# Kernel tuning notes

Hardware: AMD Instinct MI355X
Metric: run time of the kernel (lower is better)

The kernel has to match this reference:

```python
import jax, jax.numpy as jnp
import numpy as np

H = 512
T = 512
B = 32

def _gru_layer(x_tm, mask_tm, W_ih, W_hh, b_ih, b_hh):
    # x_tm: [T, B, H] time-major input; mask_tm: [T, B, 1] bool (t < length)
    # Precompute input projections for all timesteps: [T, B, 3H]
    x_proj = jnp.einsum('tbi,gi->tbg', x_tm, W_ih) + b_ih

    def step(h, inp):
        xp, m = inp                      # xp: [B,3H], m: [B,1]
        hp = h @ W_hh.T + b_hh           # [B,3H]
        xr, xz, xn = jnp.split(xp, 3, axis=-1)
        hr, hz, hn = jnp.split(hp, 3, axis=-1)
        r = jax.nn.sigmoid(xr + hr)
        z = jax.nn.sigmoid(xz + hz)
        n = jnp.tanh(xn + r * hn)
        h_new = (1.0 - z) * n + z * h
        # packed-sequence semantics: hidden frozen past length, output zero past length
        h = jnp.where(m, h_new, h)
        y = jnp.where(m, h_new, jnp.zeros_like(h_new))
        return h, y

    h0 = jnp.zeros((x_tm.shape[1], W_hh.shape[1]), x_tm.dtype)
    _, ys = jax.lax.scan(step, h0, (x_proj, mask_tm))
    return ys  # [T, B, H]


def setup_inputs() -> dict:
    key = jax.random.key(0)
    ks = jax.random.split(key, 12)
    edu_hidden = jax.random.normal(ks[0], (B, T, H), dtype=jnp.float32)
    edu_lengths = jax.random.randint(ks[1], (B,), 1, T + 1)
    edu_lengths = edu_lengths.at[0].set(T)  # pad_packed output length == T
    s = 1.0 / np.sqrt(H)
    def U(k, shape):
        return jax.random.uniform(k, shape, jnp.float32, -s, s)
    return {
        'edu_hidden': edu_hidden,
        'edu_lengths': edu_lengths,
        'W_ih_0': U(ks[2], (3 * H, H)), 'W_hh_0': U(ks[3], (3 * H, H)),
        'b_ih_0': U(ks[4], (3 * H,)),   'b_hh_0': U(ks[5], (3 * H,)),
        'W_ih_1': U(ks[6], (3 * H, H)), 'W_hh_1': U(ks[7], (3 * H, H)),
        'b_ih_1': U(ks[8], (3 * H,)),   'b_hh_1': U(ks[9], (3 * H,)),
    }


def reference(edu_hidden, edu_lengths, W_ih_0, W_hh_0, b_ih_0, b_hh_0,
              W_ih_1, W_hh_1, b_ih_1, b_hh_1):
    # mask[t, b] = t < edu_lengths[b]
    t_idx = jnp.arange(T)
    mask_tm = (t_idx[:, None] < edu_lengths[None, :])[:, :, None]  # [T, B, 1]
    x = jnp.transpose(edu_hidden, (1, 0, 2))  # time-major [T, B, H]
    x = _gru_layer(x, mask_tm, W_ih_0, W_hh_0, b_ih_0, b_hh_0)
    x = _gru_layer(x, mask_tm, W_ih_1, W_hh_1, b_ih_1, b_hh_1)
    return jnp.transpose(x, (1, 0, 2))  # [B, T, H], zeros past each length
```

## Files before the change

kernel.cpp:

```cpp
#include <hip/hip_runtime.h>
#include <cstdint>
#include <cstddef>

#define Hdim 512
#define Tdim 512
#define Bdim 32
#define NWG  256
#define SCAN_THREADS 384

typedef float        f32x4 __attribute__((ext_vector_type(4)));
typedef unsigned int u32x4 __attribute__((ext_vector_type(4)));
typedef unsigned int u32x2 __attribute__((ext_vector_type(2)));

__device__ __forceinline__ float sigmoidf_(float v) {
    return 1.f / (1.f + __expf(-v));
}
__device__ __forceinline__ float tanhf_(float a) {
    float ax = fabsf(a);
    float e  = __expf(-2.f * ax);
    float t  = (1.f - e) / (1.f + e);
    return copysignf(t, a);
}

__global__ void __launch_bounds__(SCAN_THREADS, 1)
gru_scan(const float* __restrict__ xp,
         const float* __restrict__ Whh,
         const float* __restrict__ bhh,
         const int*   __restrict__ lens,
         float*       __restrict__ y,
         u32x2*       hb2,
         int t0, int Tc)
{
    __shared__ float  hlf[4 * Hdim];
    __shared__ float4 part4[16 * 49];
    __shared__ float  dummy_guard[4];

    const int tid = threadIdx.x;
    const int wg  = blockIdx.x;
    const int u   = wg & 31;
    const int bg  = wg >> 5;
    const int j0  = u << 4;
    const int b0  = bg << 2;
    const int rp  = tid >> 4;
    const int kq  = tid & 15;

    float4 w0[8], w1[8];
    {
        int g0 = ((rp >> 4) << 9) + j0 + (rp & 15);
        int r1 = rp + 24;
        int g1 = ((r1 >> 4) << 9) + j0 + (r1 & 15);
        const float* p0 = Whh + ((size_t)g0 << 9) + (kq << 5);
        const float* p1 = Whh + ((size_t)g1 << 9) + (kq << 5);
#pragma unroll
        for (int i = 0; i < 8; ++i) {
            w0[i] = *(const float4*)(p0 + (i << 2));
            w1[i] = *(const float4*)(p1 + (i << 2));
        }
    }

    const bool isGate = tid < 64;
    const int gjl = tid & 15;
    const int gb  = (tid >> 4) & 3;
    const int jg  = j0 + gjl;
    int   glen = 0;
    float bh_r = 0.f, bh_z = 0.f, bh_n = 0.f;
    int holdIdx = 0;
    const float* xpb = nullptr;
    if (isGate) {
        glen = lens[b0 + gb];
        bh_r = bhh[jg];
        bh_z = bhh[512 + jg];
        bh_n = bhh[1024 + jg];
        int L = jg >> 2, c = jg & 3;
        int P = L ^ ((L >> 3) & 7);
        holdIdx = (gb << 9) + (P << 2) + c;
        xpb = xp + (size_t)(b0 + gb) * Tc * 1536;
    }

    const bool isPoll = tid < 256;
    const int  pb  = tid >> 6;
    const int  pL  = (tid & 63) << 1;
    const int  pP0 = pL ^ ((pL >> 3) & 7);
    const int  pP1 = pP0 ^ 1;
    float* lds_w0 = &hlf[(pb << 9) + (pP0 << 2)];
    float* lds_w1 = &hlf[(pb << 9) + (pP1 << 2)];

    float xr = 0.f, xz = 0.f, xn = 0.f;
    if (isGate) {
        xr = xpb[jg];
        xz = xpb[512 + jg];
        xn = xpb[1024 + jg];
    }

    int budget = 1 << 20;

    for (int t = t0; t < t0 + Tc; ++t) {
        const unsigned tg = (unsigned)t;

        if (isPoll) {
            const u32x2* src = hb2 + ((size_t)(t & 1) << 14) + (bg << 11) + (tid << 3);
            u32x4 q0, q1, q2, q3;
            for (;;) {
                asm volatile(
                    "global_load_dwordx4 %0, %4, off sc0 sc1\n\t"
                    "global_load_dwordx4 %1, %4, off offset:16 sc0 sc1\n\t"
                    "global_load_dwordx4 %2, %4, off offset:32 sc0 sc1\n\t"
                    "global_load_dwordx4 %3, %4, off offset:48 sc0 sc1\n\t"
                    "s_waitcnt vmcnt(0)"
                    : "=&v"(q0), "=&v"(q1), "=&v"(q2), "=&v"(q3)
                    : "v"(src) : "memory");
                bool ok = (q0[1] == tg) & (q0[3] == tg) & (q1[1] == tg) & (q1[3] == tg) &
                          (q2[1] == tg) & (q2[3] == tg) & (q3[1] == tg) & (q3[3] == tg);
                if (__all(ok)) break;
                if (--budget < 0) break;
            }
            f32x4 h0 = { __uint_as_float(q0[0]), __uint_as_float(q0[2]),
                         __uint_as_float(q1[0]), __uint_as_float(q1[2]) };
            f32x4 h1 = { __uint_as_float(q2[0]), __uint_as_float(q2[2]),
                         __uint_as_float(q3[0]), __uint_as_float(q3[2]) };
            *(f32x4*)lds_w0 = h0;
            *(f32x4*)lds_w1 = h1;
        }
        float xrn = 0.f, xzn = 0.f, xnn = 0.f;
        if (isGate) {
            int tf = (t + 1 < t0 + Tc) ? (t + 1 - t0) : (t - t0);
            const float* xq = xpb + (size_t)tf * 1536;
            xrn = xq[jg];
            xzn = xq[512 + jg];
            xnn = xq[1024 + jg];
        }
        __syncthreads();

        float acc0[4], acc1[4];
#pragma unroll
        for (int b = 0; b < 4; ++b) {
            const float4* hb = (const float4*)&hlf[b << 9];
            float a0 = 0.f, a1 = 0.f;
#pragma unroll
            for (int i = 0; i < 8; ++i) {
                float4 h = hb[(kq << 3) + (i ^ (kq & 7))];
                a0 = fmaf(w0[i].x, h.x, a0);
                a0 = fmaf(w0[i].y, h.y, a0);
                a0 = fmaf(w0[i].z, h.z, a0);
                a0 = fmaf(w0[i].w, h.w, a0);
                a1 = fmaf(w1[i].x, h.x, a1);
                a1 = fmaf(w1[i].y, h.y, a1);
                a1 = fmaf(w1[i].z, h.z, a1);
                a1 = fmaf(w1[i].w, h.w, a1);
            }
            acc0[b] = a0; acc1[b] = a1;
        }
        part4[kq * 49 + rp]      = make_float4(acc0[0], acc0[1], acc0[2], acc0[3]);
        part4[kq * 49 + rp + 24] = make_float4(acc1[0], acc1[1], acc1[2], acc1[3]);
        __syncthreads();

        if (isGate) {
            const float* part = (const float*)part4;
            float s0 = 0.f, s1 = 0.f, s2 = 0.f;
#pragma unroll
            for (int k = 0; k < 16; ++k) {
                const float* pp = part + (k * 49) * 4;
                s0 += pp[(gjl << 2) + gb];
                s1 += pp[((16 + gjl) << 2) + gb];
                s2 += pp[((32 + gjl) << 2) + gb];
            }
            float hold = hlf[holdIdx];
            float rg = sigmoidf_(xr + s0 + bh_r);
            float zg = sigmoidf_(xz + s1 + bh_z);
            float ng = tanhf_(xn + rg * (s2 + bh_n));
            float hnew = (1.f - zg) * ng + zg * hold;
            bool m = t < glen;
            float hnext = m ? hnew : hold;
            y[((size_t)(b0 + gb) * Tdim + t) * Hdim + jg] = m ? hnew : 0.f;
            u32x2 pv;
            pv[0] = __float_as_uint(hnext);
            pv[1] = (unsigned)(t + 1);
            u32x2* dst = hb2 + ((size_t)((t + 1) & 1) << 14) + (bg << 11) + (gb << 9) + jg;
            asm volatile("global_store_dwordx2 %0, %1, off sc0 sc1"
                         :: "v"(dst), "v"(pv) : "memory");
            xr = xrn; xz = xzn; xn = xnn;
        }
        __syncthreads();
    }
}

#define FMA4(c, a, b) { (c).x = fmaf((a), (b).x, (c).x); (c).y = fmaf((a), (b).y, (c).y); \
                        (c).z = fmaf((a), (b).z, (c).z); (c).w = fmaf((a), (b).w, (c).w); }

__global__ void __launch_bounds__(256)
gemm_xproj(const float* __restrict__ A,
           const float* __restrict__ W,
           const float* __restrict__ bias,
           float* __restrict__ C,
           int tcLog, int t0)
{
    __shared__ float As[16][132];
    __shared__ float Bs[16][132];
    const int tid = threadIdx.x;
    const int n0  = blockIdx.x << 7;
    const int m0  = blockIdx.y << 7;
    const int tx  = tid & 15;
    const int ty  = tid >> 4;

    const int mrow = tid >> 2;
    const int kcol = (tid & 3) << 2;
    const int Tcm1 = (1 << tcLog) - 1;

    int mg0 = m0 + mrow;
    int mg1 = m0 + 64 + mrow;
    size_t srow0 = (size_t)(mg0 >> tcLog) * Tdim + t0 + (mg0 & Tcm1);
    size_t srow1 = (size_t)(mg1 >> tcLog) * Tdim + t0 + (mg1 & Tcm1);
    const float* Ap0 = A + srow0 * Hdim + kcol;
    const float* Ap1 = A + srow1 * Hdim + kcol;
    const float* Wp0 = W + (size_t)(n0 + mrow) * Hdim + kcol;
    const float* Wp1 = W + (size_t)(n0 + 64 + mrow) * Hdim + kcol;

    float4 c00[4], c01[4], c10[4], c11[4];
#pragma unroll
    for (int i = 0; i < 4; ++i) {
        c00[i] = {0.f,0.f,0.f,0.f}; c01[i] = {0.f,0.f,0.f,0.f};
        c10[i] = {0.f,0.f,0.f,0.f}; c11[i] = {0.f,0.f,0.f,0.f};
    }

    float4 a0 = *(const float4*)(Ap0);
    float4 a1 = *(const float4*)(Ap1);
    float4 b0 = *(const float4*)(Wp0);
    float4 b1 = *(const float4*)(Wp1);

    for (int kt = 0; kt < 512; kt += 16) {
        __syncthreads();
        As[kcol+0][mrow] = a0.x; As[kcol+1][mrow] = a0.y;
        As[kcol+2][mrow] = a0.z; As[kcol+3][mrow] = a0.w;
        As[kcol+0][mrow+64] = a1.x; As[kcol+1][mrow+64] = a1.y;
        As[kcol+2][mrow+64] = a1.z; As[kcol+3][mrow+64] = a1.w;
        Bs[kcol+0][mrow] = b0.x; Bs[kcol+1][mrow] = b0.y;
        Bs[kcol+2][mrow] = b0.z; Bs[kcol+3][mrow] = b0.w;
        Bs[kcol+0][mrow+64] = b1.x; Bs[kcol+1][mrow+64] = b1.y;
        Bs[kcol+2][mrow+64] = b1.z; Bs[kcol+3][mrow+64] = b1.w;
        __syncthreads();
        if (kt + 16 < 512) {
            a0 = *(const float4*)(Ap0 + kt + 16);
            a1 = *(const float4*)(Ap1 + kt + 16);
            b0 = *(const float4*)(Wp0 + kt + 16);
            b1 = *(const float4*)(Wp1 + kt + 16);
        }
#pragma unroll
        for (int kk = 0; kk < 16; ++kk) {
            float4 aA = *(const float4*)&As[kk][ty * 4];
            float4 aB = *(const float4*)&As[kk][64 + ty * 4];
            float4 bA = *(const float4*)&Bs[kk][tx * 4];
            float4 bB = *(const float4*)&Bs[kk][64 + tx * 4];
            FMA4(c00[0], aA.x, bA); FMA4(c01[0], aA.x, bB);
            FMA4(c00[1], aA.y, bA); FMA4(c01[1], aA.y, bB);
            FMA4(c00[2], aA.z, bA); FMA4(c01[2], aA.z, bB);
            FMA4(c00[3], aA.w, bA); FMA4(c01[3], aA.w, bB);
            FMA4(c10[0], aB.x, bA); FMA4(c11[0], aB.x, bB);
            FMA4(c10[1], aB.y, bA); FMA4(c11[1], aB.y, bB);
            FMA4(c10[2], aB.z, bA); FMA4(c11[2], aB.z, bB);
            FMA4(c10[3], aB.w, bA); FMA4(c11[3], aB.w, bB);
        }
    }

    float4 biasA = *(const float4*)(bias + n0 + tx * 4);
    float4 biasB = *(const float4*)(bias + n0 + 64 + tx * 4);
#pragma unroll
    for (int i = 0; i < 4; ++i) {
        size_t row0 = (size_t)m0 + ty * 4 + i;
        size_t row1 = row0 + 64;
        float4 v;
        v.x = c00[i].x + biasA.x; v.y = c00[i].y + biasA.y;
        v.z = c00[i].z + biasA.z; v.w = c00[i].w + biasA.w;
        *(float4*)(C + row0 * 1536 + n0 + tx * 4) = v;
        v.x = c01[i].x + biasB.x; v.y = c01[i].y + biasB.y;
        v.z = c01[i].z + biasB.z; v.w = c01[i].w + biasB.w;
        *(float4*)(C + row0 * 1536 + n0 + 64 + tx * 4) = v;
        v.x = c10[i].x + biasA.x; v.y = c10[i].y + biasA.y;
        v.z = c10[i].z + biasA.z; v.w = c10[i].w + biasA.w;
        *(float4*)(C + row1 * 1536 + n0 + tx * 4) = v;
        v.x = c11[i].x + biasB.x; v.y = c11[i].y + biasB.y;
        v.z = c11[i].z + biasB.z; v.w = c11[i].w + biasB.w;
        *(float4*)(C + row1 * 1536 + n0 + 64 + tx * 4) = v;
    }
}

extern "C" void kernel_launch(void* const* d_in, const int* in_sizes, int n_in,
                              void* d_out, int out_size, void* d_ws, size_t ws_size,
                              hipStream_t stream) {
    (void)in_sizes; (void)n_in; (void)out_size;
    const float* x    = (const float*)d_in[0];
    const int*   lens = (const int*)d_in[1];
    const float* Wih0 = (const float*)d_in[2];
    const float* Whh0 = (const float*)d_in[3];
    const float* bih0 = (const float*)d_in[4];
    const float* bhh0 = (const float*)d_in[5];
    const float* Wih1 = (const float*)d_in[6];
    const float* Whh1 = (const float*)d_in[7];
    const float* bih1 = (const float*)d_in[8];
    const float* bhh1 = (const float*)d_in[9];
    float* out = (float*)d_out;

    const size_t hb2_bytes  = (size_t)2 * 8 * 2048 * 8;
    const size_t ctrl_bytes = 2 * hb2_bytes;
    int Tc = 512;
    while (Tc > 4 && (size_t)Bdim * Tc * 1536 * 4 + ctrl_bytes > ws_size) Tc >>= 1;
    int tcLog = 31 - __builtin_clz((unsigned)Tc);
    size_t xp_bytes = (size_t)Bdim * Tc * 1536 * 4;

    float* xp = (float*)d_ws;
    char*  ctrl = (char*)d_ws + xp_bytes;
    u32x2* hb2_0 = (u32x2*)ctrl;
    u32x2* hb2_1 = (u32x2*)(ctrl + hb2_bytes);

    (void)hipMemsetAsync(ctrl, 0, ctrl_bytes, stream);

    const int nChunks = Tdim / Tc;
    for (int layer = 0; layer < 2; ++layer) {
        const float* src  = layer ? (const float*)out : x;
        const float* Wih  = layer ? Wih1 : Wih0;
        const float* bih  = layer ? bih1 : bih0;
        const float* Whh  = layer ? Whh1 : Whh0;
        const float* bhhp = layer ? bhh1 : bhh0;
        u32x2* hb2 = layer ? hb2_1 : hb2_0;

        for (int c = 0; c < nChunks; ++c) {
            int t0 = c * Tc;
            dim3 gg(12, (Bdim * Tc) >> 7);
            gemm_xproj<<<gg, dim3(256), 0, stream>>>(src, Wih, bih, xp, tcLog, t0);

            const float* a_xp  = xp;
            const float* a_whh = Whh;
            const float* a_bhh = bhhp;
            const int*   a_ln  = lens;
            float*       a_y   = out;
            u32x2*       a_hb  = hb2;
            int a_t0 = t0;
            int a_tc = Tc;
            void* args[] = { &a_xp, &a_whh, &a_bhh, &a_ln, &a_y, &a_hb, &a_t0, &a_tc };
            (void)hipLaunchCooperativeKernel((const void*)gru_scan, dim3(NWG),
                                             dim3(SCAN_THREADS), args, 0, stream);
        }
    }
}
```

Measured before the change: 3.656 ms.

## Restructure recurrent matvec partitioning with wave shuffle reduction and unswizzled LDS

```diff
diff --git a/kernel.cpp b/kernel.cpp
--- a/kernel.cpp
+++ b/kernel.cpp
@@ -32,8 +32,7 @@
          int t0, int Tc)
 {
     __shared__ float  hlf[4 * Hdim];
-    __shared__ float4 part4[16 * 49];
-    __shared__ float  dummy_guard[4];
+    __shared__ float4 part4[8 * 49];
 
     const int tid = threadIdx.x;
     const int wg  = blockIdx.x;
@@ -41,21 +40,16 @@
     const int bg  = wg >> 5;
     const int j0  = u << 4;
     const int b0  = bg << 2;
-    const int rp  = tid >> 4;
-    const int kq  = tid & 15;
-
-    float4 w0[8], w1[8];
-    {
-        int g0 = ((rp >> 4) << 9) + j0 + (rp & 15);
-        int r1 = rp + 24;
-        int g1 = ((r1 >> 4) << 9) + j0 + (r1 & 15);
-        const float* p0 = Whh + ((size_t)g0 << 9) + (kq << 5);
-        const float* p1 = Whh + ((size_t)g1 << 9) + (kq << 5);
-#pragma unroll
-        for (int i = 0; i < 8; ++i) {
-            w0[i] = *(const float4*)(p0 + (i << 2));
-            w1[i] = *(const float4*)(p1 + (i << 2));
-        }
+    const int rw  = tid >> 5;
+    const int kq  = tid & 31;
+
+    float4 w[4][4];
+#pragma unroll
+    for (int i = 0; i < 4; ++i) {
+        int r = rw + 12 * i;
+        const float* p = Whh + ((size_t)(((r >> 4) << 9) + j0 + (r & 15)) << 9) + (kq << 2);
+#pragma unroll
+        for (int c = 0; c < 4; ++c) w[i][c] = *(const float4*)(p + (c << 7));
     }
 
     const bool isGate = tid < 64;
@@ -64,26 +58,20 @@
     const int jg  = j0 + gjl;
     int   glen = 0;
     float bh_r = 0.f, bh_z = 0.f, bh_n = 0.f;
-    int holdIdx = 0;
     const float* xpb = nullptr;
     if (isGate) {
         glen = lens[b0 + gb];
         bh_r = bhh[jg];
         bh_z = bhh[512 + jg];
         bh_n = bhh[1024 + jg];
-        int L = jg >> 2, c = jg & 3;
-        int P = L ^ ((L >> 3) & 7);
-        holdIdx = (gb << 9) + (P << 2) + c;
         xpb = xp + (size_t)(b0 + gb) * Tc * 1536;
     }
 
     const bool isPoll = tid < 256;
     const int  pb  = tid >> 6;
     const int  pL  = (tid & 63) << 1;
-    const int  pP0 = pL ^ ((pL >> 3) & 7);
-    const int  pP1 = pP0 ^ 1;
-    float* lds_w0 = &hlf[(pb << 9) + (pP0 << 2)];
-    float* lds_w1 = &hlf[(pb << 9) + (pP1 << 2)];
+    float* lds_w0 = &hlf[(pb << 9) + (pL << 2)];
+    float* lds_w1 = lds_w0 + 4;
 
     float xr = 0.f, xz = 0.f, xn = 0.f;
     if (isGate) {
@@ -131,47 +119,66 @@
         }
         __syncthreads();
 
-        float acc0[4], acc1[4];
+        float acc[4][4];
+#pragma unroll
+        for (int i = 0; i < 4; ++i)
+#pragma unroll
+            for (int b = 0; b < 4; ++b) acc[i][b] = 0.f;
 #pragma unroll
         for (int b = 0; b < 4; ++b) {
-            const float4* hb = (const float4*)&hlf[b << 9];
-            float a0 = 0.f, a1 = 0.f;
-#pragma unroll
-            for (int i = 0; i < 8; ++i) {
-                float4 h = hb[(kq << 3) + (i ^ (kq & 7))];
-                a0 = fmaf(w0[i].x, h.x, a0);
-                a0 = fmaf(w0[i].y, h.y, a0);
-                a0 = fmaf(w0[i].z, h.z, a0);
-                a0 = fmaf(w0[i].w, h.w, a0);
-                a1 = fmaf(w1[i].x, h.x, a1);
-                a1 = fmaf(w1[i].y, h.y, a1);
-                a1 = fmaf(w1[i].z, h.z, a1);
-                a1 = fmaf(w1[i].w, h.w, a1);
+            const float4* hb4 = (const float4*)&hlf[b << 9];
+            float4 h0 = hb4[kq];
+            float4 h1 = hb4[kq + 32];
+            float4 h2 = hb4[kq + 64];
+            float4 h3 = hb4[kq + 96];
+#pragma unroll
+            for (int i = 0; i < 4; ++i) {
+                float a = acc[i][b];
+                a = fmaf(w[i][0].x, h0.x, a); a = fmaf(w[i][0].y, h0.y, a);
+                a = fmaf(w[i][0].z, h0.z, a); a = fmaf(w[i][0].w, h0.w, a);
+                a = fmaf(w[i][1].x, h1.x, a); a = fmaf(w[i][1].y, h1.y, a);
+                a = fmaf(w[i][1].z, h1.z, a); a = fmaf(w[i][1].w, h1.w, a);
+                a = fmaf(w[i][2].x, h2.x, a); a = fmaf(w[i][2].y, h2.y, a);
+                a = fmaf(w[i][2].z, h2.z, a); a = fmaf(w[i][2].w, h2.w, a);
+                a = fmaf(w[i][3].x, h3.x, a); a = fmaf(w[i][3].y, h3.y, a);
+                a = fmaf(w[i][3].z, h3.z, a); a = fmaf(w[i][3].w, h3.w, a);
+                acc[i][b] = a;
             }
-            acc0[b] = a0; acc1[b] = a1;
-        }
-        part4[kq * 49 + rp]      = make_float4(acc0[0], acc0[1], acc0[2], acc0[3]);
-        part4[kq * 49 + rp + 24] = make_float4(acc1[0], acc1[1], acc1[2], acc1[3]);
+        }
+#pragma unroll
+        for (int mm = 1; mm <= 2; mm <<= 1)
+#pragma unroll
+            for (int i = 0; i < 4; ++i)
+#pragma unroll
+                for (int b = 0; b < 4; ++b)
+                    acc[i][b] += __shfl_xor(acc[i][b], mm);
+        if ((kq & 3) == 0) {
+            int mp = kq >> 2;
+#pragma unroll
+            for (int i = 0; i < 4; ++i)
+                part4[mp * 49 + rw + 12 * i] =
+                    make_float4(acc[i][0], acc[i][1], acc[i][2], acc[i][3]);
+        }
         __syncthreads();
 
         if (isGate) {
-            const float* part = (const float*)part4;
+            const float* pf = (const float*)part4;
             float s0 = 0.f, s1 = 0.f, s2 = 0.f;
 #pragma unroll
-            for (int k = 0; k < 16; ++k) {
-                const float* pp = part + (k * 49) * 4;
-                s0 += pp[(gjl << 2) + gb];
-                s1 += pp[((16 + gjl) << 2) + gb];
-                s2 += pp[((32 + gjl) << 2) + gb];
+            for (int m = 0; m < 8; ++m) {
+                int base = ((m * 49 + gjl) << 2) + gb;
+                s0 += pf[base];
+                s1 += pf[base + 64];
+                s2 += pf[base + 128];
             }
-            float hold = hlf[holdIdx];
-            float rg = sigmoidf_(xr + s0 + bh_r);
-            float zg = sigmoidf_(xz + s1 + bh_z);
-            float ng = tanhf_(xn + rg * (s2 + bh_n));
-            float hnew = (1.f - zg) * ng + zg * hold;
-            bool m = t < glen;
-            float hnext = m ? hnew : hold;
-            y[((size_t)(b0 + gb) * Tdim + t) * Hdim + jg] = m ? hnew : 0.f;
+            float hold = hlf[(gb << 9) + jg];
+            float rr = sigmoidf_(xr + s0 + bh_r);
+            float zz = sigmoidf_(xz + s1 + bh_z);
+            float nn = tanhf_(xn + rr * (s2 + bh_n));
+            float hnew = (1.f - zz) * nn + zz * hold;
+            bool msk = t < glen;
+            float hnext = msk ? hnew : hold;
+            y[((size_t)(b0 + gb) * Tdim + t) * Hdim + jg] = msk ? hnew : 0.f;
             u32x2 pv;
             pv[0] = __float_as_uint(hnext);
             pv[1] = (unsigned)(t + 1);
```

Measured after the change: 3.717 ms. No clear change (+1.6%).
